# Kernel tuning notes

Hardware: AMD Instinct MI355X
Metric: run time of the kernel (lower is better)

## Reference

```python
import jax, jax.numpy as jnp
import numpy as np

N_EMBD = 2048
N_HEAD = 16
KV_GROUP = 4
HEAD_DIM = N_EMBD // N_HEAD          # 128
N_KV = N_HEAD // KV_GROUP            # 4
KV_DIM = N_KV * HEAD_DIM             # 512
B, T = 2, 2048
ROPE_THETA = 1000000.0


def setup_inputs() -> dict:
    key = jax.random.key(0)
    k0, k1, k2 = jax.random.split(key, 3)
    x = jax.random.normal(k0, (B, T, N_EMBD), dtype=jnp.float32)
    # weights stored (in, out); matches torch Linear math up to a transpose of random init
    W_attn = jax.random.normal(k1, (N_EMBD, N_EMBD + 2 * KV_DIM), dtype=jnp.float32) * 0.02
    b_attn = jnp.zeros((N_EMBD + 2 * KV_DIM,), dtype=jnp.float32)
    W_proj = jax.random.normal(k2, (N_EMBD, N_EMBD), dtype=jnp.float32) * 0.02
    # realistic RoPE frequencies (Qwen-style theta)
    inv_freq = 1.0 / (ROPE_THETA ** (np.arange(0, HEAD_DIM, 2, dtype=np.float64) / HEAD_DIM))
    ang = np.outer(np.arange(T, dtype=np.float64), inv_freq)  # (T, HEAD_DIM//2)
    freqs_cos = jnp.asarray(np.cos(ang), dtype=jnp.float32)
    freqs_sin = jnp.asarray(np.sin(ang), dtype=jnp.float32)
    return {"x": x, "W_attn": W_attn, "b_attn": b_attn, "W_proj": W_proj,
            "freqs_cos": freqs_cos, "freqs_sin": freqs_sin}


def _rope_expand(x, cos, sin, kv_group):
    # x: (B, T, n_kv, hd); complex rotate interleaved pairs, then expand to n_kv*kv_group heads
    Bx, Tx, nh, hd = x.shape
    xf = x.astype(jnp.float32).reshape(Bx, Tx, nh, hd // 2, 2)
    a, b = xf[..., 0], xf[..., 1]
    c = cos[None, :, None, :]  # (1, T, 1, hd//2)
    s = sin[None, :, None, :]
    yr = a * c - b * s
    yi = a * s + b * c
    y = jnp.stack([yr, yi], axis=-1).reshape(Bx, Tx, nh, hd)
    y = jnp.broadcast_to(y[:, :, :, None, :], (Bx, Tx, nh, kv_group, hd))
    return y.reshape(Bx, Tx, nh * kv_group, hd).astype(x.dtype)


def reference(x, W_attn, b_attn, W_proj, freqs_cos, freqs_sin):
    Bx, Tx, E = x.shape
    hd = 2 * freqs_cos.shape[-1]
    n_q = E // hd
    kv_dim = (W_attn.shape[1] - E) // 2
    n_kv = kv_dim // hd
    g = n_q // n_kv

    qkv = x @ W_attn + b_attn  # (B, T, E + 2*kv_dim)
    q = qkv[..., :E].reshape(Bx, Tx, n_q, hd).transpose(0, 2, 1, 3)          # bhtd
    k = qkv[..., E:E + kv_dim].reshape(Bx, Tx, n_kv, hd)
    v = qkv[..., E + kv_dim:].reshape(Bx, Tx, n_kv, hd)
    # faithful to source: RoPE on K AND V (not Q), then GQA expand
    k = _rope_expand(k, freqs_cos, freqs_sin, g).transpose(0, 2, 1, 3)       # bhtd
    v = _rope_expand(v, freqs_cos, freqs_sin, g).transpose(0, 2, 1, 3)       # bhtd

    scale = 1.0 / jnp.sqrt(jnp.asarray(hd, dtype=x.dtype))
    scores = jnp.einsum('bhqd,bhkd->bhqk', q, k) * scale                     # (B, H, T, T)
    causal = jnp.tril(jnp.ones((Tx, Tx), dtype=bool))
    scores = jnp.where(causal, scores, jnp.asarray(-jnp.inf, scores.dtype))
    attn = jax.nn.softmax(scores, axis=-1)
    y = jnp.einsum('bhqk,bhkd->bhqd', attn, v)
    y = y.transpose(0, 2, 1, 3).reshape(Bx, Tx, E)
    return y @ W_proj  # c_proj, no bias
```

## Files before the change

### kernel.cpp

```cpp
#include <hip/hip_runtime.h>
#include <cstdint>
#include <cstddef>

#define T_SEQ 2048
#define B_SZ  2
#define EMB   2048
#define NH    16
#define NKV   4
#define HD    128
#define KVD   512
#define QKVN  3072
#define MROWS (B_SZ*T_SEQ)

typedef __bf16 bf16x8 __attribute__((ext_vector_type(8)));
typedef float  f32x4  __attribute__((ext_vector_type(4)));
typedef short  s16x8  __attribute__((ext_vector_type(8)));
typedef unsigned short u16;

__device__ __forceinline__ u16 f2b(float f) {
  uint32_t u = __builtin_bit_cast(uint32_t, f);
  u += 0x7fffu + ((u >> 16) & 1u);
  return (u16)(u >> 16);
}
__device__ __forceinline__ float b2f(u16 h) {
  return __builtin_bit_cast(float, (uint32_t)h << 16);
}
__device__ __forceinline__ bf16x8 ld_bf8(const u16* p) {
  return __builtin_bit_cast(bf16x8, *(const s16x8*)p);
}
__device__ __forceinline__ void glds16(const void* g, void* l) {
  __builtin_amdgcn_global_load_lds((const __attribute__((address_space(1))) void*)g,
                                   (__attribute__((address_space(3))) void*)l, 16, 0, 0);
}
template<int N> __device__ __forceinline__ void waitv() {
  if constexpr (N == 0) asm volatile("s_waitcnt vmcnt(0)" ::: "memory");
  else if constexpr (N == 2) asm volatile("s_waitcnt vmcnt(2)" ::: "memory");
  else if constexpr (N == 3) asm volatile("s_waitcnt vmcnt(3)" ::: "memory");
  __builtin_amdgcn_sched_barrier(0);
}

#define CVT_BLKS (MROWS*EMB/4/256)
#define TW1_BX   (QKVN/64)
#define TW1_BLKS (TW1_BX*(EMB/64))
__global__ void prep_kernel(const float4* __restrict__ x, ushort4* __restrict__ xb,
                            const float* __restrict__ Wa, u16* __restrict__ WaT) {
  __shared__ float tile[64][65];
  const int bid = blockIdx.x, tid = threadIdx.x;
  if (bid < CVT_BLKS) {
    int i = bid*256 + tid;
    float4 v = x[i];
    ushort4 o;
    o.x = f2b(v.x); o.y = f2b(v.y); o.z = f2b(v.z); o.w = f2b(v.w);
    xb[i] = o;
    return;
  }
  const int tb = bid - CVT_BLKS;
  const int C = QKVN, R = EMB;
  const int c0 = (tb % TW1_BX)*64, r0 = (tb / TW1_BX)*64;
  const int tx = tid & 15, ty = tid >> 4;
#pragma unroll
  for (int k = 0; k < 4; ++k) {
    int r = ty + k*16;
    float4 v = *(const float4*)&Wa[(size_t)(r0+r)*C + c0 + tx*4];
    tile[r][tx*4+0] = v.x; tile[r][tx*4+1] = v.y;
    tile[r][tx*4+2] = v.z; tile[r][tx*4+3] = v.w;
  }
  __syncthreads();
#pragma unroll
  for (int k = 0; k < 4; ++k) {
    int c = ty + k*16;
    ushort4 o;
    o.x = f2b(tile[tx*4+0][c]);
    o.y = f2b(tile[tx*4+1][c]);
    o.z = f2b(tile[tx*4+2][c]);
    o.w = f2b(tile[tx*4+3][c]);
    *(ushort4*)&WaT[(size_t)(c0+c)*R + r0 + tx*4] = o;
  }
}

template<int BN, int WGN, int MF, int NF, int NF1, int SB, int SB1, int VMC, bool BF16_OUT>
__global__ __launch_bounds__(512, 2) void gemm_kernel(const u16* __restrict__ A,
        const u16* __restrict__ Bt, const float* __restrict__ bias,
        void* __restrict__ Cout, int M, int N, int K) {
  constexpr int MF2 = MF/2;
  __shared__ u16 As[2][256*64];
  __shared__ u16 Bs[2][BN*64];
  const int tid = threadIdx.x;
  const int w = tid >> 6, lane = tid & 63;
  const int quad = lane >> 4, lc = lane & 15;
  const int wrow = w / WGN, wcol = w % WGN;
  const int gx = gridDim.x;
  const int lin = blockIdx.y*gx + blockIdx.x;
  const int swz = (lin & 7)*32 + (lin >> 3);
  const int m0 = (swz / gx)*256, n0 = (swz % gx)*BN;

  f32x4 acc[MF][NF] = {};
  bf16x8 af[MF2][2], bfv[NF][2];

  int xoff[2];
#pragma unroll
  for (int ks = 0; ks < 2; ++ks) xoff[ks] = ((ks*4 + quad) ^ (lc & 7))*8;
  const int arow0 = (wrow*MF*16 + lc)*64;
  const int brow0 = (wcol*NF*16 + lc)*64;

  const int srb  = tid >> 3;
  const int spos = (tid & 7) ^ (srb & 7);
  const u16* sAp = A  + (size_t)(m0 + srb)*K + spos*8;
  const u16* sBp = Bt + (size_t)(n0 + srb)*K + spos*8;

#define STAGE_A(bf_, t_, h_) do { \
    glds16(sAp + (size_t)((h_)*2  )*64*K + (size_t)(t_)*64, &As[bf_][((h_)*2  )*4096 + w*512]); \
    glds16(sAp + (size_t)((h_)*2+1)*64*K + (size_t)(t_)*64, &As[bf_][((h_)*2+1)*4096 + w*512]); \
  } while (0)
#define STAGE_B(bf_, t_, p_) do { \
    _Pragma("unroll") for (int r = (p_) ? SB1 : 0; r < ((p_) ? SB : SB1); ++r) \
      glds16(sBp + (size_t)r*64*K + (size_t)(t_)*64, &Bs[bf_][r*4096 + w*512]); \
  } while (0)
#define LDAH(S_, h_) do { _Pragma("unroll") for (int i = 0; i < MF2; ++i) { \
    af[i][0] = ld_bf8((S_) + arow0 + ((h_)*MF2 + i)*1024 + xoff[0]); \
    af[i][1] = ld_bf8((S_) + arow0 + ((h_)*MF2 + i)*1024 + xoff[1]); } } while (0)
#define LDBG(S_, g_) do { _Pragma("unroll") for (int j = (g_) ? NF1 : 0; j < ((g_) ? NF : NF1); ++j) { \
    bfv[j][0] = ld_bf8((S_) + brow0 + j*1024 + xoff[0]); \
    bfv[j][1] = ld_bf8((S_) + brow0 + j*1024 + xoff[1]); } } while (0)
#define CL(h_, g_) do { _Pragma("unroll") for (int ks = 0; ks < 2; ++ks) \
    _Pragma("unroll") for (int i = 0; i < MF2; ++i) \
    _Pragma("unroll") for (int j = (g_) ? NF1 : 0; j < ((g_) ? NF : NF1); ++j) \
      acc[(h_)*MF2+i][j] = __builtin_amdgcn_mfma_f32_16x16x32_bf16( \
          af[i][ks], bfv[j][ks], acc[(h_)*MF2+i][j], 0, 0, 0); } while (0)
#define BARX()  __builtin_amdgcn_s_barrier()
#define SCHB()  __builtin_amdgcn_sched_barrier(0)
#define MFMAPH(h_, g_) do { BARX(); \
    asm volatile("s_waitcnt lgkmcnt(0)" ::: "memory"); SCHB(); \
    __builtin_amdgcn_s_setprio(1); CL(h_, g_); __builtin_amdgcn_s_setprio(0); \
  } while (0)

  const int NT = K >> 6;
  STAGE_B(0, 0, 0); STAGE_B(0, 0, 1);
  STAGE_A(0, 0, 0); STAGE_A(0, 0, 1);
  STAGE_B(1, 1, 0); STAGE_B(1, 1, 1);
  waitv<VMC>();
  BARX(); SCHB();

  for (int t0 = 0; t0 < NT-2; t0 += 2) {
    const u16 *a0 = As[0], *b0 = Bs[0], *a1 = As[1], *b1 = Bs[1];
    LDAH(a0, 0); LDBG(b0, 0); STAGE_A(1, t0+1, 0);
    MFMAPH(0, 0); BARX();
    LDBG(b0, 1); STAGE_A(1, t0+1, 1);
    MFMAPH(0, 1); BARX();
    LDAH(a0, 1); STAGE_B(0, t0+2, 0);
    MFMAPH(1, 0); BARX();
    STAGE_B(0, t0+2, 1);
    MFMAPH(1, 1);
    waitv<VMC>();
    BARX(); SCHB();
    LDAH(a1, 0); LDBG(b1, 0); STAGE_A(0, t0+2, 0);
    MFMAPH(0, 0); BARX();
    LDBG(b1, 1); STAGE_A(0, t0+2, 1);
    MFMAPH(0, 1); BARX();
    LDAH(a1, 1); STAGE_B(1, t0+3, 0);
    MFMAPH(1, 0); BARX();
    STAGE_B(1, t0+3, 1);
    MFMAPH(1, 1);
    waitv<VMC>();
    BARX(); SCHB();
  }
  {
    const u16 *a0 = As[0], *b0 = Bs[0], *a1 = As[1], *b1 = Bs[1];
    LDAH(a0, 0); LDBG(b0, 0); STAGE_A(1, NT-1, 0);
    MFMAPH(0, 0); BARX();
    LDBG(b0, 1); STAGE_A(1, NT-1, 1);
    MFMAPH(0, 1); BARX();
    LDAH(a0, 1);
    MFMAPH(1, 0); BARX();
    MFMAPH(1, 1);
    waitv<0>();
    BARX(); SCHB();
    LDAH(a1, 0); LDBG(b1, 0);
    MFMAPH(0, 0); BARX();
    LDBG(b1, 1);
    MFMAPH(0, 1); BARX();
    LDAH(a1, 1);
    MFMAPH(1, 0); BARX();
    MFMAPH(1, 1);
  }

#undef STAGE_A
#undef STAGE_B
#undef LDAH
#undef LDBG
#undef CL
#undef BARX
#undef SCHB
#undef MFMAPH

#pragma unroll
  for (int j = 0; j < NF; ++j) {
    int col = n0 + wcol*NF*16 + j*16 + lc;
    float bv = BF16_OUT ? bias[col] : 0.0f;
#pragma unroll
    for (int i = 0; i < MF; ++i) {
      int rowb = m0 + wrow*MF*16 + i*16 + quad*4;
#pragma unroll
      for (int r = 0; r < 4; ++r) {
        float v = acc[i][j][r] + bv;
        if (BF16_OUT) ((u16*)Cout)[(size_t)(rowb+r)*N + col] = f2b(v);
        else          ((float*)Cout)[(size_t)(rowb+r)*N + col] = v;
      }
    }
  }
}

#define RTV_BLKS (8*(T_SEQ/32))
#define TW2_BX   (EMB/64)
__global__ void ropetv_kernel(const u16* __restrict__ qkv, const float* __restrict__ fc,
                              const float* __restrict__ fs, u16* __restrict__ kout,
                              u16* __restrict__ vtb, const float* __restrict__ Wp,
                              u16* __restrict__ WpT) {
  __shared__ float tile[64][65];
  __shared__ u16 vt[32][136];
  const int bid = blockIdx.x, tid = threadIdx.x;
  if (bid < RTV_BLKS) {
    const int bkv = bid & 7;
    const int t0 = (bid >> 3)*32;
    const int b = bkv >> 2, kv = bkv & 3;
    const int tl = tid >> 3, ch = tid & 7;
    const int t = t0 + tl;
    const int row = b*T_SEQ + t;
    const u16* p = qkv + (size_t)row*QKVN + EMB + kv*HD + ch*16;
    s16x8 kin0 = *(const s16x8*)p,        kin1 = *(const s16x8*)(p + 8);
    s16x8 vin0 = *(const s16x8*)(p + KVD), vin1 = *(const s16x8*)(p + KVD + 8);
    s16x8 ko0, ko1, vo0, vo1;
#pragma unroll
    for (int j = 0; j < 4; ++j) {
      int i = ch*8 + j;
      float c = fc[t*64 + i], s = fs[t*64 + i];
      float ka = b2f((u16)kin0[2*j]), kb2 = b2f((u16)kin0[2*j+1]);
      float va = b2f((u16)vin0[2*j]), vb2 = b2f((u16)vin0[2*j+1]);
      ko0[2*j]   = (short)f2b(ka*c - kb2*s);
      ko0[2*j+1] = (short)f2b(ka*s + kb2*c);
      vo0[2*j]   = (short)f2b(va*c - vb2*s);
      vo0[2*j+1] = (short)f2b(va*s + vb2*c);
    }
#pragma unroll
    for (int j = 0; j < 4; ++j) {
      int i = ch*8 + 4 + j;
      float c = fc[t*64 + i], s = fs[t*64 + i];
      float ka = b2f((u16)kin1[2*j]), kb2 = b2f((u16)kin1[2*j+1]);
      float va = b2f((u16)vin1[2*j]), vb2 = b2f((u16)vin1[2*j+1]);
      ko1[2*j]   = (short)f2b(ka*c - kb2*s);
      ko1[2*j+1] = (short)f2b(ka*s + kb2*c);
      vo1[2*j]   = (short)f2b(va*c - vb2*s);
      vo1[2*j+1] = (short)f2b(va*s + vb2*c);
    }
    u16* kq = kout + (size_t)row*KVD + kv*HD + ch*16;
    *(s16x8*)kq       = ko0;
    *(s16x8*)(kq + 8) = ko1;
    *(s16x8*)&vt[tl][ch*16]     = vo0;
    *(s16x8*)&vt[tl][ch*16 + 8] = vo1;
    __syncthreads();
    const int d = tid >> 1, hf = tid & 1;
    u16 ov[16];
#pragma unroll
    for (int e = 0; e < 16; ++e) ov[e] = vt[hf*16 + e][d];
    u16* vq = vtb + (size_t)(bkv*HD + d)*T_SEQ + t0 + hf*16;
    *(s16x8*)vq       = *(s16x8*)&ov[0];
    *(s16x8*)(vq + 8) = *(s16x8*)&ov[8];
    return;
  }
  const int tb = bid - RTV_BLKS;
  const int C = EMB, R = EMB;
  const int c0 = (tb % TW2_BX)*64, r0 = (tb / TW2_BX)*64;
  const int tx = tid & 15, ty = tid >> 4;
#pragma unroll
  for (int k = 0; k < 4; ++k) {
    int r = ty + k*16;
    float4 v = *(const float4*)&Wp[(size_t)(r0+r)*C + c0 + tx*4];
    tile[r][tx*4+0] = v.x; tile[r][tx*4+1] = v.y;
    tile[r][tx*4+2] = v.z; tile[r][tx*4+3] = v.w;
  }
  __syncthreads();
#pragma unroll
  for (int k = 0; k < 4; ++k) {
    int c = ty + k*16;
    ushort4 o;
    o.x = f2b(tile[tx*4+0][c]);
    o.y = f2b(tile[tx*4+1][c]);
    o.z = f2b(tile[tx*4+2][c]);
    o.w = f2b(tile[tx*4+3][c]);
    *(ushort4*)&WpT[(size_t)(c0+c)*R + r0 + tx*4] = o;
  }
}

__global__ __launch_bounds__(256, 2) void flash_kernel(const u16* __restrict__ qkv,
    const u16* __restrict__ kb, const u16* __restrict__ vtb, u16* __restrict__ yb) {
  __shared__ u16 Ks[2][64*128];
  __shared__ u16 Vs[2][128*64];
  __shared__ u16 Ps[4][16*64];
  const int tid = threadIdx.x;
  const int w = tid >> 6, lane = tid & 63;
  const int quad = lane >> 4, lc = lane & 15;
  const int bkv = blockIdx.x & 7;
  const int r_  = blockIdx.x >> 3;
  const int b = bkv >> 2, kv = bkv & 3;
  const int h = kv*4 + w;
  const int qbase = (127 - r_)*16;

  bf16x8 qf[4];
  {
    const u16* qp = qkv + (size_t)(b*T_SEQ + qbase + lc)*QKVN + h*HD + quad*8;
#pragma unroll
    for (int ks = 0; ks < 4; ++ks) qf[ks] = ld_bf8(qp + ks*32);
  }

  f32x4 o[8] = {};
  float rs[4] = {0.f, 0.f, 0.f, 0.f};
  const u16* kbase = kb  + (size_t)b*T_SEQ*KVD + kv*HD;
  const u16* vbase = vtb + (size_t)bkv*HD*T_SEQ;
  const int nk = qbase + 16;
  const int nt = (nk + 63) >> 6;
  const float cs = 0.08838834764831845f * 1.4426950408889634f;
  u16* pw = Ps[w];

  const u16* kptr[4];
  const u16* vptr[4];
#pragma unroll
  for (int rr = 0; rr < 4; ++rr) {
    int krow = (rr*4 + w)*4 + (lane >> 4);
    int kcc  = (lane & 15) ^ (krow & 15);
    kptr[rr] = kbase + (size_t)krow*KVD + kcc*8;
    int vrow = (rr*4 + w)*8 + (lane >> 3);
    int vcc  = (lane & 7) ^ (vrow & 7);
    vptr[rr] = vbase + (size_t)vrow*T_SEQ + vcc*8;
  }

  int koff[4], voff[2], poff[2];
#pragma unroll
  for (int ks = 0; ks < 4; ++ks) koff[ks] = lc*128 + (((ks*4 + quad) ^ lc)*8);
#pragma unroll
  for (int ks = 0; ks < 2; ++ks) voff[ks] = lc*64 + (((ks*4 + quad) ^ (lc & 7))*8);
#pragma unroll
  for (int ks = 0; ks < 2; ++ks) poff[ks] = lc*64 + (((ks*4 + quad) ^ (lc & 7))*8);
  int pwb[4], pwx[4];
#pragma unroll
  for (int r = 0; r < 4; ++r) {
    pwb[r] = (quad*4 + r)*64 + (lc & 7);
    pwx[r] = (quad*4 + r) & 7;
  }
  const int pcc = lc >> 3;

#pragma unroll
  for (int rr = 0; rr < 4; ++rr) glds16(kptr[rr], &Ks[0][(rr*4 + w)*512]);
#pragma unroll
  for (int rr = 0; rr < 4; ++rr) glds16(vptr[rr], &Vs[0][(rr*4 + w)*512]);
  asm volatile("s_waitcnt vmcnt(0)" ::: "memory");
  __builtin_amdgcn_sched_barrier(0);
  __builtin_amdgcn_s_barrier();
  __builtin_amdgcn_sched_barrier(0);

  for (int t = 0; t < nt; ++t) {
    const int cur = t & 1;
    if (t + 1 < nt) {
#pragma unroll
      for (int rr = 0; rr < 4; ++rr)
        glds16(kptr[rr] + (size_t)(t+1)*64*KVD, &Ks[cur^1][(rr*4 + w)*512]);
#pragma unroll
      for (int rr = 0; rr < 4; ++rr)
        glds16(vptr[rr] + (size_t)(t+1)*64,     &Vs[cur^1][(rr*4 + w)*512]);
    }
    const u16* ksb = Ks[cur];
    const u16* vsb = Vs[cur];
    const int k0 = t*64;

    f32x4 sc[4] = {};
    __builtin_amdgcn_s_setprio(1);
#pragma unroll
    for (int nt2 = 0; nt2 < 4; ++nt2)
#pragma unroll
      for (int ks = 0; ks < 4; ++ks) {
        bf16x8 kf = ld_bf8(ksb + nt2*16*128 + koff[ks]);
        sc[nt2] = __builtin_amdgcn_mfma_f32_16x16x32_bf16(qf[ks], kf, sc[nt2], 0, 0, 0);
      }
    __builtin_amdgcn_s_setprio(0);

    if (k0 + 63 > qbase) {
#pragma unroll
      for (int nt2 = 0; nt2 < 4; ++nt2) {
        int key = k0 + nt2*16 + lc;
        int qrow = qbase + quad*4;
#pragma unroll
        for (int r = 0; r < 4; ++r) {
          float e = __builtin_amdgcn_exp2f(sc[nt2][r]*cs);
          float p = (key <= qrow + r) ? e : 0.0f;
          rs[r] += p;
          pw[pwb[r] + ((nt2*2 + pcc) ^ pwx[r])*8] = f2b(p);
        }
      }
    } else {
#pragma unroll
      for (int nt2 = 0; nt2 < 4; ++nt2)
#pragma unroll
        for (int r = 0; r < 4; ++r) {
          float p = __builtin_amdgcn_exp2f(sc[nt2][r]*cs);
          rs[r] += p;
          pw[pwb[r] + ((nt2*2 + pcc) ^ pwx[r])*8] = f2b(p);
        }
    }

    bf16x8 pa[2];
#pragma unroll
    for (int ks = 0; ks < 2; ++ks)
      pa[ks] = ld_bf8(pw + poff[ks]);

    __builtin_amdgcn_s_setprio(1);
#pragma unroll
    for (int j = 0; j < 8; ++j)
#pragma unroll
      for (int ks = 0; ks < 2; ++ks) {
        bf16x8 vf = ld_bf8(vsb + j*16*64 + voff[ks]);
        o[j] = __builtin_amdgcn_mfma_f32_16x16x32_bf16(pa[ks], vf, o[j], 0, 0, 0);
      }
    __builtin_amdgcn_s_setprio(0);

    asm volatile("s_waitcnt vmcnt(0)" ::: "memory");
    __builtin_amdgcn_sched_barrier(0);
    __builtin_amdgcn_s_barrier();
    __builtin_amdgcn_sched_barrier(0);
  }

#pragma unroll
  for (int r = 0; r < 4; ++r) {
    float v = rs[r];
#pragma unroll
    for (int off2 = 8; off2 >= 1; off2 >>= 1)
      v += __shfl_xor(v, off2);
    float inv = 1.0f / v;
    size_t orow = (size_t)(b*T_SEQ + qbase + quad*4 + r)*EMB + h*HD;
#pragma unroll
    for (int j = 0; j < 8; ++j)
      yb[orow + j*16 + lc] = f2b(o[j][r]*inv);
  }
}

extern "C" void kernel_launch(void* const* d_in, const int* in_sizes, int n_in,
                              void* d_out, int out_size, void* d_ws, size_t ws_size,
                              hipStream_t stream) {
  const float* x      = (const float*)d_in[0];
  const float* W_attn = (const float*)d_in[1];
  const float* b_attn = (const float*)d_in[2];
  const float* W_proj = (const float*)d_in[3];
  const float* fc     = (const float*)d_in[4];
  const float* fs     = (const float*)d_in[5];

  u16* ws   = (u16*)d_ws;
  u16* xb   = ws;
  u16* WaT  = xb   + (size_t)MROWS*EMB;
  u16* qkv  = WaT  + (size_t)QKVN*EMB;
  u16* kbuf = qkv  + (size_t)MROWS*QKVN;
  u16* vtb  = kbuf + (size_t)MROWS*KVD;
  u16* WpT  = WaT;
  u16* yb   = xb;
  float* out = (float*)d_out;

  prep_kernel<<<CVT_BLKS + TW1_BLKS, 256, 0, stream>>>(
      (const float4*)x, (ushort4*)xb, W_attn, WaT);
  gemm_kernel<192, 4, 8, 3, 2, 3, 2, 3, true>
      <<<dim3(QKVN/192, MROWS/256), 512, 0, stream>>>(
      xb, WaT, b_attn, qkv, MROWS, QKVN, EMB);
  ropetv_kernel<<<RTV_BLKS + TW2_BX*(EMB/64), 256, 0, stream>>>(
      qkv, fc, fs, kbuf, vtb, W_proj, WpT);
  flash_kernel<<<dim3(B_SZ*NKV*(T_SEQ/16)), 256, 0, stream>>>(qkv, kbuf, vtb, yb);
  gemm_kernel<128, 2, 4, 4, 2, 2, 1, 2, false>
      <<<dim3(EMB/128, MROWS/256), 512, 0, stream>>>(
      yb, WpT, nullptr, out, MROWS, EMB, EMB);
}
```

Measured before the change: 278.8 us.

## Restructure GEMM main loop into two MFMA phases with fixed 2x4 wave grid

The bf16 GEMM main loop now runs two MFMA phases per k-tile instead of four, which halves the barrier and lgkm-wait points. Each phase loads all B fragments at once and reorders the global-to-LDS staging of A halves and B tiles, with matching vmcnt waits. The wave grid is fixed at 2x4, so the output projection GEMM changes from 64x64 to 128x32 per-wave tiles. This cuts synchronisation overhead but gives less overlap granularity and a different register footprint and operand reuse.

```diff
diff --git a/kernel.cpp b/kernel.cpp
--- a/kernel.cpp
+++ b/kernel.cpp
@@ -34,8 +34,8 @@
 }
 template<int N> __device__ __forceinline__ void waitv() {
   if constexpr (N == 0) asm volatile("s_waitcnt vmcnt(0)" ::: "memory");
-  else if constexpr (N == 2) asm volatile("s_waitcnt vmcnt(2)" ::: "memory");
-  else if constexpr (N == 3) asm volatile("s_waitcnt vmcnt(3)" ::: "memory");
+  else if constexpr (N == 4) asm volatile("s_waitcnt vmcnt(4)" ::: "memory");
+  else if constexpr (N == 5) asm volatile("s_waitcnt vmcnt(5)" ::: "memory");
   __builtin_amdgcn_sched_barrier(0);
 }
 
@@ -78,29 +78,28 @@
   }
 }
 
-template<int BN, int WGN, int MF, int NF, int NF1, int SB, int SB1, int VMC, bool BF16_OUT>
+template<int BN, int NF, int SB, int VMC, bool BF16_OUT>
 __global__ __launch_bounds__(512, 2) void gemm_kernel(const u16* __restrict__ A,
         const u16* __restrict__ Bt, const float* __restrict__ bias,
         void* __restrict__ Cout, int M, int N, int K) {
-  constexpr int MF2 = MF/2;
   __shared__ u16 As[2][256*64];
   __shared__ u16 Bs[2][BN*64];
   const int tid = threadIdx.x;
   const int w = tid >> 6, lane = tid & 63;
   const int quad = lane >> 4, lc = lane & 15;
-  const int wrow = w / WGN, wcol = w % WGN;
+  const int wrow = w >> 2, wcol = w & 3;
   const int gx = gridDim.x;
   const int lin = blockIdx.y*gx + blockIdx.x;
   const int swz = (lin & 7)*32 + (lin >> 3);
   const int m0 = (swz / gx)*256, n0 = (swz % gx)*BN;
 
-  f32x4 acc[MF][NF] = {};
-  bf16x8 af[MF2][2], bfv[NF][2];
+  f32x4 acc[8][NF] = {};
+  bf16x8 af[4][2], bfv[NF][2];
 
   int xoff[2];
 #pragma unroll
   for (int ks = 0; ks < 2; ++ks) xoff[ks] = ((ks*4 + quad) ^ (lc & 7))*8;
-  const int arow0 = (wrow*MF*16 + lc)*64;
+  const int arow0 = (wrow*128 + lc)*64;
   const int brow0 = (wcol*NF*16 + lc)*64;
 
   const int srb  = tid >> 3;
@@ -108,87 +107,72 @@
   const u16* sAp = A  + (size_t)(m0 + srb)*K + spos*8;
   const u16* sBp = Bt + (size_t)(n0 + srb)*K + spos*8;
 
-#define STAGE_A(bf_, t_, h_) do { \
-    glds16(sAp + (size_t)((h_)*2  )*64*K + (size_t)(t_)*64, &As[bf_][((h_)*2  )*4096 + w*512]); \
-    glds16(sAp + (size_t)((h_)*2+1)*64*K + (size_t)(t_)*64, &As[bf_][((h_)*2+1)*4096 + w*512]); \
+#define STAGE_AH(bf_, t_, h_) do { \
+    glds16(sAp + (size_t)(h_)*64*K     + (size_t)(t_)*64, &As[bf_][(h_)*4096 + w*512]); \
+    glds16(sAp + (size_t)((h_)+2)*64*K + (size_t)(t_)*64, &As[bf_][((h_)+2)*4096 + w*512]); \
   } while (0)
-#define STAGE_B(bf_, t_, p_) do { \
-    _Pragma("unroll") for (int r = (p_) ? SB1 : 0; r < ((p_) ? SB : SB1); ++r) \
+#define STAGE_B(bf_, t_) do { \
+    _Pragma("unroll") for (int r = 0; r < SB; ++r) \
       glds16(sBp + (size_t)r*64*K + (size_t)(t_)*64, &Bs[bf_][r*4096 + w*512]); \
   } while (0)
-#define LDAH(S_, h_) do { _Pragma("unroll") for (int i = 0; i < MF2; ++i) { \
-    af[i][0] = ld_bf8((S_) + arow0 + ((h_)*MF2 + i)*1024 + xoff[0]); \
-    af[i][1] = ld_bf8((S_) + arow0 + ((h_)*MF2 + i)*1024 + xoff[1]); } } while (0)
-#define LDBG(S_, g_) do { _Pragma("unroll") for (int j = (g_) ? NF1 : 0; j < ((g_) ? NF : NF1); ++j) { \
+#define LDAH(S_, h_) do { _Pragma("unroll") for (int i = 0; i < 4; ++i) { \
+    af[i][0] = ld_bf8((S_) + arow0 + (h_)*4096 + i*1024 + xoff[0]); \
+    af[i][1] = ld_bf8((S_) + arow0 + (h_)*4096 + i*1024 + xoff[1]); } } while (0)
+#define LDBALL(S_) do { _Pragma("unroll") for (int j = 0; j < NF; ++j) { \
     bfv[j][0] = ld_bf8((S_) + brow0 + j*1024 + xoff[0]); \
     bfv[j][1] = ld_bf8((S_) + brow0 + j*1024 + xoff[1]); } } while (0)
-#define CL(h_, g_) do { _Pragma("unroll") for (int ks = 0; ks < 2; ++ks) \
-    _Pragma("unroll") for (int i = 0; i < MF2; ++i) \
-    _Pragma("unroll") for (int j = (g_) ? NF1 : 0; j < ((g_) ? NF : NF1); ++j) \
-      acc[(h_)*MF2+i][j] = __builtin_amdgcn_mfma_f32_16x16x32_bf16( \
-          af[i][ks], bfv[j][ks], acc[(h_)*MF2+i][j], 0, 0, 0); } while (0)
+#define CLH(h_) do { _Pragma("unroll") for (int ks = 0; ks < 2; ++ks) \
+    _Pragma("unroll") for (int i = 0; i < 4; ++i) \
+    _Pragma("unroll") for (int j = 0; j < NF; ++j) \
+      acc[(h_)*4+i][j] = __builtin_amdgcn_mfma_f32_16x16x32_bf16( \
+          af[i][ks], bfv[j][ks], acc[(h_)*4+i][j], 0, 0, 0); } while (0)
 #define BARX()  __builtin_amdgcn_s_barrier()
 #define SCHB()  __builtin_amdgcn_sched_barrier(0)
-#define MFMAPH(h_, g_) do { BARX(); \
+#define MFMAPH(h_) do { BARX(); \
     asm volatile("s_waitcnt lgkmcnt(0)" ::: "memory"); SCHB(); \
-    __builtin_amdgcn_s_setprio(1); CL(h_, g_); __builtin_amdgcn_s_setprio(0); \
+    __builtin_amdgcn_s_setprio(1); CLH(h_); __builtin_amdgcn_s_setprio(0); \
   } while (0)
 
   const int NT = K >> 6;
-  STAGE_B(0, 0, 0); STAGE_B(0, 0, 1);
-  STAGE_A(0, 0, 0); STAGE_A(0, 0, 1);
-  STAGE_B(1, 1, 0); STAGE_B(1, 1, 1);
+  STAGE_AH(0, 0, 0); STAGE_AH(0, 0, 1); STAGE_B(0, 0);
+  STAGE_AH(1, 1, 0); STAGE_B(1, 1);
   waitv<VMC>();
   BARX(); SCHB();
 
   for (int t0 = 0; t0 < NT-2; t0 += 2) {
     const u16 *a0 = As[0], *b0 = Bs[0], *a1 = As[1], *b1 = Bs[1];
-    LDAH(a0, 0); LDBG(b0, 0); STAGE_A(1, t0+1, 0);
-    MFMAPH(0, 0); BARX();
-    LDBG(b0, 1); STAGE_A(1, t0+1, 1);
-    MFMAPH(0, 1); BARX();
-    LDAH(a0, 1); STAGE_B(0, t0+2, 0);
-    MFMAPH(1, 0); BARX();
-    STAGE_B(0, t0+2, 1);
-    MFMAPH(1, 1);
+    LDAH(a0, 0); LDBALL(b0); STAGE_AH(1, t0+1, 1);
+    MFMAPH(0); BARX();
+    LDAH(a0, 1); STAGE_B(0, t0+2); STAGE_AH(0, t0+2, 0);
+    MFMAPH(1);
     waitv<VMC>();
     BARX(); SCHB();
-    LDAH(a1, 0); LDBG(b1, 0); STAGE_A(0, t0+2, 0);
-    MFMAPH(0, 0); BARX();
-    LDBG(b1, 1); STAGE_A(0, t0+2, 1);
-    MFMAPH(0, 1); BARX();
-    LDAH(a1, 1); STAGE_B(1, t0+3, 0);
-    MFMAPH(1, 0); BARX();
-    STAGE_B(1, t0+3, 1);
-    MFMAPH(1, 1);
+    LDAH(a1, 0); LDBALL(b1); STAGE_AH(0, t0+2, 1);
+    MFMAPH(0); BARX();
+    LDAH(a1, 1); STAGE_B(1, t0+3); STAGE_AH(1, t0+3, 0);
+    MFMAPH(1);
     waitv<VMC>();
     BARX(); SCHB();
   }
   {
     const u16 *a0 = As[0], *b0 = Bs[0], *a1 = As[1], *b1 = Bs[1];
-    LDAH(a0, 0); LDBG(b0, 0); STAGE_A(1, NT-1, 0);
-    MFMAPH(0, 0); BARX();
-    LDBG(b0, 1); STAGE_A(1, NT-1, 1);
-    MFMAPH(0, 1); BARX();
+    LDAH(a0, 0); LDBALL(b0); STAGE_AH(1, NT-1, 1);
+    MFMAPH(0); BARX();
     LDAH(a0, 1);
-    MFMAPH(1, 0); BARX();
-    MFMAPH(1, 1);
+    MFMAPH(1);
     waitv<0>();
     BARX(); SCHB();
-    LDAH(a1, 0); LDBG(b1, 0);
-    MFMAPH(0, 0); BARX();
-    LDBG(b1, 1);
-    MFMAPH(0, 1); BARX();
+    LDAH(a1, 0); LDBALL(b1);
+    MFMAPH(0); BARX();
     LDAH(a1, 1);
-    MFMAPH(1, 0); BARX();
-    MFMAPH(1, 1);
-  }
-
-#undef STAGE_A
+    MFMAPH(1);
+  }
+
+#undef STAGE_AH
 #undef STAGE_B
 #undef LDAH
-#undef LDBG
-#undef CL
+#undef LDBALL
+#undef CLH
 #undef BARX
 #undef SCHB
 #undef MFMAPH
@@ -198,8 +182,8 @@
     int col = n0 + wcol*NF*16 + j*16 + lc;
     float bv = BF16_OUT ? bias[col] : 0.0f;
 #pragma unroll
-    for (int i = 0; i < MF; ++i) {
-      int rowb = m0 + wrow*MF*16 + i*16 + quad*4;
+    for (int i = 0; i < 8; ++i) {
+      int rowb = m0 + wrow*128 + i*16 + quad*4;
 #pragma unroll
       for (int r = 0; r < 4; ++r) {
         float v = acc[i][j][r] + bv;
@@ -463,13 +447,13 @@
 
   prep_kernel<<<CVT_BLKS + TW1_BLKS, 256, 0, stream>>>(
       (const float4*)x, (ushort4*)xb, W_attn, WaT);
-  gemm_kernel<192, 4, 8, 3, 2, 3, 2, 3, true>
+  gemm_kernel<192, 3, 3, 5, true>
       <<<dim3(QKVN/192, MROWS/256), 512, 0, stream>>>(
       xb, WaT, b_attn, qkv, MROWS, QKVN, EMB);
   ropetv_kernel<<<RTV_BLKS + TW2_BX*(EMB/64), 256, 0, stream>>>(
       qkv, fc, fs, kbuf, vtb, W_proj, WpT);
   flash_kernel<<<dim3(B_SZ*NKV*(T_SEQ/16)), 256, 0, stream>>>(qkv, kbuf, vtb, yb);
-  gemm_kernel<128, 2, 4, 4, 2, 2, 1, 2, false>
+  gemm_kernel<128, 2, 2, 4, false>
       <<<dim3(EMB/128, MROWS/256), 512, 0, stream>>>(
       yb, WpT, nullptr, out, MROWS, EMB, EMB);
 }
```

Result: faster. 268.6 us (-3.6%).
